# Performance work log

Measured on AMD Instinct MI355X. Metric: run time of the kernel, lower is better.

The kernel has to match this reference:

```python
import jax, jax.numpy as jnp
import numpy as np

B, CIN, H, W = 16, 256, 56, 56
D, HEADS, KS, PAD, STRIDE, M = 256, 8, 3, 1, 1, 4
K = KS * KS
N = D // HEADS
# relative_indices: sum of window coords, flattened row-major, values in [0, 2*KS-2]
REL = (np.arange(KS)[:, None] + np.arange(KS)[None, :]).reshape(-1)


def setup_inputs() -> dict:
    key = jax.random.key(0)
    ks = jax.random.split(key, 7)
    return {
        "x": jax.random.normal(ks[0], (B, CIN, H, W), jnp.float32),
        "q": jax.random.normal(ks[1], (B, D, 1), jnp.float32),
        "Wk": jax.random.normal(ks[2], (D, CIN), jnp.float32) * 0.05,
        "Wv": jax.random.normal(ks[3], (D, CIN), jnp.float32) * 0.05,
        "pos_emb": jax.random.normal(ks[4], (1, 2 * KS - 1), jnp.float32),
        "Wlin": jax.random.normal(ks[5], (1, M), jnp.float32),
        "Wproj": jax.random.normal(ks[6], (D, D), jnp.float32) * 0.05,
    }


def _unfold(t):
    # torch nn.Unfold: (B,C,H,W) -> (B, C*K, L); patches feature dim ordered (C, kh, kw)
    p = jax.lax.conv_general_dilated_patches(
        t, (KS, KS), (STRIDE, STRIDE), [(PAD, PAD), (PAD, PAD)])
    b, _, ho, wo = p.shape
    return p.reshape(b, -1, ho * wo), ho, wo


def reference(x, q, Wk, Wv, pos_emb, Wlin, Wproj):
    b = x.shape[0]
    k = jnp.einsum('oc,bchw->bohw', Wk, x)  # 1x1 conv, no bias
    v = jnp.einsum('oc,bchw->bohw', Wv, x)
    ku, ho, wo = _unfold(k)
    vu, _, _ = _unfold(v)
    L = ho * wo
    ku = ku.reshape(b, HEADS, N, K, L)  # (b, h, n, k, l)
    vu = vu.reshape(b, HEADS, N, K, L)
    qh = q.reshape(b, HEADS, N)  # learned per-batch query, d=1 squeezed
    attn = jnp.einsum('bhn,bhnkl->bhlk', qh, ku)  # (b,h,l,K)
    attn = attn + pos_emb[0, REL]  # relative position bias, shape (K,)
    attn = jax.nn.softmax(attn, axis=-1)
    # repeat d(=1) -> m identical rows then Linear(m,1,no bias): equals scale by sum(Wlin)
    attn = attn * jnp.sum(Wlin)
    out = jnp.einsum('bhlk,bhnkl->bhnl', attn, vu)  # (b,h,n,l)
    out = out.reshape(b, D, ho, wo)  # fold with kernel 1 == reshape
    return jnp.einsum('oc,bchw->bohw', Wproj, out)  # 1x1 proj conv
```

## Files before the change

### kernel.cpp

```cpp
#include <hip/hip_runtime.h>

#define B_     16
#define D_     256
#define HEADS_ 8
#define N_     32
#define H_     56
#define W_     56
#define L_     3136
#define BL_    (B_ * L_)

typedef short short8 __attribute__((ext_vector_type(8)));
typedef float f32x4  __attribute__((ext_vector_type(4)));

__device__ __forceinline__ unsigned short f2bf(float f) {
    union { float f; unsigned u; } c; c.f = f;
    unsigned u = c.u;
    u += 0x7fffu + ((u >> 16) & 1u);
    return (unsigned short)(u >> 16);
}

#define GL2L(g, l) __builtin_amdgcn_global_load_lds( \
    (const __attribute__((address_space(1))) void*)(g), \
    (__attribute__((address_space(3))) void*)(l), 16, 0, 0)

__global__ __launch_bounds__(256) void convert_w_kernel(
    const float* __restrict__ Wv, const float* __restrict__ Wproj,
    const float* __restrict__ Wk, const float* __restrict__ q,
    unsigned short* __restrict__ Wvb, unsigned short* __restrict__ Wpb,
    float* __restrict__ qt)
{
    if (blockIdx.y < 2) {
        const float* src   = (blockIdx.y == 0) ? Wv  : Wproj;
        unsigned short* dst = (blockIdx.y == 0) ? Wvb : Wpb;
        const int i = (blockIdx.x * 256 + threadIdx.x) * 4;
        float4 v = *(const float4*)(src + i);
        uint2 o;
        o.x = (unsigned)f2bf(v.x) | ((unsigned)f2bf(v.y) << 16);
        o.y = (unsigned)f2bf(v.z) | ((unsigned)f2bf(v.w) << 16);
        *(uint2*)(dst + i) = o;
    } else {
        const int b  = blockIdx.x >> 2;
        const int h0 = (blockIdx.x & 3) * 2;
        const int c  = threadIdx.x;
#pragma unroll
        for (int hh = 0; hh < 2; ++hh) {
            const int h = h0 + hh;
            const float* qb = q  + b * D_ + h * N_;
            const float* wr = Wk + (size_t)(h * N_) * D_ + c;
            float acc = 0.f;
#pragma unroll 8
            for (int n = 0; n < N_; ++n)
                acc = fmaf(qb[n], wr[(size_t)n * D_], acc);
            qt[((size_t)b * HEADS_ + h) * D_ + c] = acc;
        }
    }
}

__global__ __launch_bounds__(256) void transpose_s_kernel(
    const float* __restrict__ x, const float* __restrict__ qt,
    unsigned short* __restrict__ Xt, float* __restrict__ S)
{
    __shared__ float tile[64][65];
    __shared__ float qs[2048];
    __shared__ float Sred[4][8][64];

    const int bb = blockIdx.z;
    const int l0 = blockIdx.x * 64;
    const int t  = threadIdx.x;
    const int g4 = (t & 15) * 4;
    const int rr = t >> 4;
    const int sl = t & 63;
    const int cq = t >> 6;

    {
        const float4* s4 = (const float4*)(qt + (size_t)bb * HEADS_ * D_);
        ((float4*)qs)[t]       = s4[t];
        ((float4*)qs)[t + 256] = s4[t + 256];
    }

    float sacc[8];
#pragma unroll
    for (int h = 0; h < 8; ++h) sacc[h] = 0.f;

    const float* xb = x + ((size_t)bb * D_) * L_ + l0;
    unsigned short* Xb = Xt + ((size_t)bb * L_ + l0) * D_;

    for (int ct = 0; ct < 4; ++ct) {
        const int c0 = ct * 64;
        float4 v[4];
#pragma unroll
        for (int i = 0; i < 4; ++i)
            v[i] = *(const float4*)(xb + (size_t)(c0 + rr + i * 16) * L_ + g4);
        __syncthreads();
#pragma unroll
        for (int i = 0; i < 4; ++i)
            *(float4*)&tile[rr + i * 16][g4] = v[i];
        __syncthreads();

#pragma unroll
        for (int i = 0; i < 4; ++i) {
            const int l = rr + i * 16;
            uint2 o;
            o.x = (unsigned)f2bf(tile[g4 + 0][l]) | ((unsigned)f2bf(tile[g4 + 1][l]) << 16);
            o.y = (unsigned)f2bf(tile[g4 + 2][l]) | ((unsigned)f2bf(tile[g4 + 3][l]) << 16);
            *(uint2*)(Xb + (size_t)l * D_ + c0 + g4) = o;
        }

#pragma unroll
        for (int cc = 0; cc < 16; ++cc) {
            const float xv = tile[cq * 16 + cc][sl];
            const int  ci = c0 + cq * 16 + cc;
#pragma unroll
            for (int h = 0; h < 8; ++h)
                sacc[h] = fmaf(qs[h * 256 + ci], xv, sacc[h]);
        }
    }

    __syncthreads();
#pragma unroll
    for (int h = 0; h < 8; ++h) Sred[cq][h][sl] = sacc[h];
    __syncthreads();
    {
        const int h0 = t >> 6;
#pragma unroll
        for (int r = 0; r < 2; ++r) {
            const int h = h0 + r * 4;
            const float s = Sred[0][h][sl] + Sred[1][h][sl] + Sred[2][h][sl] + Sred[3][h][sl];
            S[((size_t)bb * HEADS_ + h) * L_ + l0 + sl] = s;
        }
    }
}

__global__ __launch_bounds__(256) void gemm_v_mfma(
    const unsigned short* __restrict__ Xt, const unsigned short* __restrict__ Wvb,
    unsigned short* __restrict__ Vo)
{
    __shared__ unsigned short As[2][128 * 32];
    __shared__ unsigned short Bs[2][128 * 32];

    const int t = threadIdx.x;
    const int w = t >> 6, lane = t & 63, col = lane & 15, quad = lane >> 4;
    const int wr = w >> 1, wc = w & 1;
    const int n0 = blockIdx.x * 128;
    const int d0 = blockIdx.y * 128;
    const int srow = t >> 2;
    const int skc  = (t & 3) * 8;

    const unsigned short* Ag = Wvb + (size_t)(d0 + srow) * D_ + skc;
    const unsigned short* Bg = Xt + (size_t)(n0 + srow) * D_ + skc;

    f32x4 acc[4][4];
#pragma unroll
    for (int m = 0; m < 4; ++m)
#pragma unroll
        for (int n = 0; n < 4; ++n) acc[m][n] = (f32x4){0.f, 0.f, 0.f, 0.f};

    {
        char* An = (char*)&As[0][0] + w * 1024;
        char* Bn = (char*)&Bs[0][0] + w * 1024;
        GL2L(Ag, An);            GL2L(Ag + 64 * D_, An + 4096);
        GL2L(Bg, Bn);            GL2L(Bg + 64 * D_, Bn + 4096);
    }
    __syncthreads();

#pragma unroll
    for (int kt = 0; kt < 8; ++kt) {
        const int cur = kt & 1;
        if (kt < 7) {
            const int c1 = (kt + 1) * 32;
            char* An = (char*)&As[cur ^ 1][0] + w * 1024;
            char* Bn = (char*)&Bs[cur ^ 1][0] + w * 1024;
            GL2L(Ag + c1, An);           GL2L(Ag + 64 * D_ + c1, An + 4096);
            GL2L(Bg + c1, Bn);           GL2L(Bg + 64 * D_ + c1, Bn + 4096);
        }
        const unsigned short* Ab = &As[cur][0];
        const unsigned short* Bb = &Bs[cur][0];
        short8 af[4], bf[4];
#pragma unroll
        for (int m = 0; m < 4; ++m)
            af[m] = *(const short8*)(Ab + (wr * 64 + m * 16 + col) * 32 + quad * 8);
#pragma unroll
        for (int n = 0; n < 4; ++n)
            bf[n] = *(const short8*)(Bb + (wc * 64 + n * 16 + col) * 32 + quad * 8);
#pragma unroll
        for (int m = 0; m < 4; ++m)
#pragma unroll
            for (int n = 0; n < 4; ++n)
                acc[m][n] = __builtin_amdgcn_mfma_f32_16x16x32_bf16(af[m], bf[n], acc[m][n], 0, 0, 0);
        __syncthreads();
    }

#pragma unroll
    for (int n = 0; n < 4; ++n) {
        const unsigned flat = n0 + wc * 64 + n * 16 + col;
        const unsigned bq = flat / L_;
        const unsigned lq = flat - bq * L_;
        unsigned short* vout = Vo + (size_t)bq * D_ * L_ + lq;
#pragma unroll
        for (int m = 0; m < 4; ++m) {
            const int dbase = d0 + wr * 64 + m * 16 + quad * 4;
#pragma unroll
            for (int r = 0; r < 4; ++r)
                vout[(size_t)(dbase + r) * L_] = f2bf(acc[m][n][r]);
        }
    }
}

__global__ __launch_bounds__(256) void attend_kernel(
    const float* __restrict__ S, const unsigned short* __restrict__ Vo,
    const float* __restrict__ pos_emb, const float* __restrict__ Wlin,
    unsigned short* __restrict__ Om)
{
    __shared__ unsigned short Vs[10][60][8];
    __shared__ float Ss[10][58];

    const int band = blockIdx.x;
    const int half = blockIdx.y;
    const int bh   = blockIdx.z;
    const int y0   = band * 8;
    const int t    = threadIdx.x;

    const float* Sb = S + (size_t)bh * L_;
    for (int wi = t; wi < 580; wi += 256) {
        const int row = wi / 58, c = wi - row * 58;
        const int gr = y0 - 1 + row, gc = c - 1;
        float v = 0.f;
        if (gr >= 0 && gr < H_ && gc >= 0 && gc < W_)
            v = Sb[gr * W_ + gc];
        Ss[row][c] = v;
    }

    const unsigned short* Vbase = Vo + ((size_t)bh * N_ + half * 8) * L_;
    for (int j = t; j < 560; j += 256) {
        const int ch = j & 7;
        const int rr = j >> 3;
        const int row = rr / 7, cg = rr - row * 7;
        const int gr = y0 - 1 + row;
        uint4 v = make_uint4(0u, 0u, 0u, 0u);
        if (gr >= 0 && gr < H_)
            v = *(const uint4*)(Vbase + (size_t)ch * L_ + gr * W_ + cg * 8);
        const unsigned short* hw = (const unsigned short*)&v;
        const int colb = cg * 8 + 1;
#pragma unroll
        for (int i = 0; i < 8; ++i)
            Vs[row][colb + i][ch] = hw[i];
    }
    if (t < 160) {
        const int row = t >> 4, side = (t >> 3) & 1, ch = t & 7;
        Vs[row][side ? 57 : 0][ch] = 0;
    }
    __syncthreads();

    const float scale = Wlin[0] + Wlin[1] + Wlin[2] + Wlin[3];
    const float pe0 = pos_emb[0], pe1 = pos_emb[1], pe2 = pos_emb[2];
    const float pe3 = pos_emb[3], pe4 = pos_emb[4];
    const float bias[9] = {pe0, pe1, pe2, pe1, pe2, pe3, pe2, pe3, pe4};

    for (int p = t; p < 448; p += 256) {
        const int yl = p / 56, xx = p - yl * 56;
        const int lr = yl + 1, lc = xx + 1;

        float lg[9], m = -1e30f;
#pragma unroll
        for (int dy = 0; dy < 3; ++dy)
#pragma unroll
            for (int dx = 0; dx < 3; ++dx) {
                const int k = dy * 3 + dx;
                lg[k] = Ss[lr - 1 + dy][lc - 1 + dx] + bias[k];
                m = fmaxf(m, lg[k]);
            }
        float ssum = 0.f;
#pragma unroll
        for (int k = 0; k < 9; ++k) { lg[k] = __expf(lg[k] - m); ssum += lg[k]; }
        const float inv = scale / ssum;

        float om[8] = {0.f, 0.f, 0.f, 0.f, 0.f, 0.f, 0.f, 0.f};
#pragma unroll
        for (int dy = 0; dy < 3; ++dy)
#pragma unroll
            for (int dx = 0; dx < 3; ++dx) {
                const float wk = lg[dy * 3 + dx] * inv;
                const uint4 v = *(const uint4*)&Vs[lr - 1 + dy][lc - 1 + dx][0];
                const unsigned* u = (const unsigned*)&v;
#pragma unroll
                for (int i = 0; i < 4; ++i) {
                    union { unsigned uu; float f; } lo, hi;
                    lo.uu = u[i] << 16;
                    hi.uu = u[i] & 0xffff0000u;
                    om[2 * i]     = fmaf(wk, lo.f, om[2 * i]);
                    om[2 * i + 1] = fmaf(wk, hi.f, om[2 * i + 1]);
                }
            }

        unsigned short ob[8];
#pragma unroll
        for (int i = 0; i < 8; ++i) ob[i] = f2bf(om[i]);
        const int l = (y0 + yl) * W_ + xx;
        *(uint4*)(Om + ((size_t)bh * L_ + l) * N_ + half * 8) = *(const uint4*)ob;
    }
}

__global__ __launch_bounds__(256) void gemm_proj_mfma(
    const unsigned short* __restrict__ Om, const unsigned short* __restrict__ Wpb,
    float* __restrict__ Out)
{
    __shared__ unsigned short As[2][128 * 32];
    __shared__ unsigned short Bs[2][128 * 32];

    const int t = threadIdx.x;
    const int w = t >> 6, lane = t & 63, col = lane & 15, quad = lane >> 4;
    const int wr = w >> 1, wc = w & 1;
    const int n0 = blockIdx.x * 128;
    const int d0 = blockIdx.y * 128;
    const int srow = t >> 2;
    const int skc  = (t & 3) * 8;

    const unsigned short* Ag = Wpb + (size_t)(d0 + srow) * D_ + skc;
    const int f0 = n0 + srow;
    const unsigned b0q = (unsigned)f0 / L_, l0q = (unsigned)f0 - b0q * L_;
    const int f1 = f0 + 64;
    const unsigned b1q = (unsigned)f1 / L_, l1q = (unsigned)f1 - b1q * L_;
    const unsigned short* Bg0 = Om + ((size_t)(b0q * HEADS_) * L_ + l0q) * N_ + skc;
    const unsigned short* Bg1 = Om + ((size_t)(b1q * HEADS_) * L_ + l1q) * N_ + skc;
    const size_t kstride = (size_t)L_ * N_;

    f32x4 acc[4][4];
#pragma unroll
    for (int m = 0; m < 4; ++m)
#pragma unroll
        for (int n = 0; n < 4; ++n) acc[m][n] = (f32x4){0.f, 0.f, 0.f, 0.f};

    {
        char* An = (char*)&As[0][0] + w * 1024;
        char* Bn = (char*)&Bs[0][0] + w * 1024;
        GL2L(Ag, An);            GL2L(Ag + 64 * D_, An + 4096);
        GL2L(Bg0, Bn);           GL2L(Bg1, Bn + 4096);
    }
    __syncthreads();

#pragma unroll
    for (int kt = 0; kt < 8; ++kt) {
        const int cur = kt & 1;
        if (kt < 7) {
            const int c1 = (kt + 1) * 32;
            char* An = (char*)&As[cur ^ 1][0] + w * 1024;
            char* Bn = (char*)&Bs[cur ^ 1][0] + w * 1024;
            GL2L(Ag + c1, An);                     GL2L(Ag + 64 * D_ + c1, An + 4096);
            GL2L(Bg0 + (kt + 1) * kstride, Bn);    GL2L(Bg1 + (kt + 1) * kstride, Bn + 4096);
        }
        const unsigned short* Ab = &As[cur][0];
        const unsigned short* Bb = &Bs[cur][0];
        short8 af[4], bf[4];
#pragma unroll
        for (int m = 0; m < 4; ++m)
            af[m] = *(const short8*)(Ab + (wr * 64 + m * 16 + col) * 32 + quad * 8);
#pragma unroll
        for (int n = 0; n < 4; ++n)
            bf[n] = *(const short8*)(Bb + (wc * 64 + n * 16 + col) * 32 + quad * 8);
#pragma unroll
        for (int m = 0; m < 4; ++m)
#pragma unroll
            for (int n = 0; n < 4; ++n)
                acc[m][n] = __builtin_amdgcn_mfma_f32_16x16x32_bf16(af[m], bf[n], acc[m][n], 0, 0, 0);
        __syncthreads();
    }

#pragma unroll
    for (int n = 0; n < 4; ++n) {
        const unsigned flat = n0 + wc * 64 + n * 16 + col;
        const unsigned bq = flat / L_;
        const unsigned lq = flat - bq * L_;
        float* oout = Out + (size_t)bq * D_ * L_ + lq;
#pragma unroll
        for (int m = 0; m < 4; ++m) {
            const int dbase = d0 + wr * 64 + m * 16 + quad * 4;
#pragma unroll
            for (int r = 0; r < 4; ++r)
                oout[(size_t)(dbase + r) * L_] = acc[m][n][r];
        }
    }
}

extern "C" void kernel_launch(void* const* d_in, const int* in_sizes, int n_in,
                              void* d_out, int out_size, void* d_ws, size_t ws_size,
                              hipStream_t stream)
{
    const float* x       = (const float*)d_in[0];
    const float* q       = (const float*)d_in[1];
    const float* Wk      = (const float*)d_in[2];
    const float* Wv      = (const float*)d_in[3];
    const float* pos_emb = (const float*)d_in[4];
    const float* Wlin    = (const float*)d_in[5];
    const float* Wproj   = (const float*)d_in[6];
    float* out = (float*)d_out;

    const size_t planeE = (size_t)B_ * D_ * L_;
    unsigned short* Xt  = (unsigned short*)d_ws;
    unsigned short* Vo  = Xt + planeE;
    unsigned short* Om  = Vo + planeE;
    unsigned short* Wvb = Om + planeE;
    unsigned short* Wpb = Wvb + D_ * D_;
    float*          S   = (float*)(Wpb + D_ * D_);
    float*          qt  = S + (size_t)B_ * HEADS_ * L_;

    convert_w_kernel<<<dim3(64, 3), 256, 0, stream>>>(Wv, Wproj, Wk, q, Wvb, Wpb, qt);
    transpose_s_kernel<<<dim3(49, 1, 16), 256, 0, stream>>>(x, qt, Xt, S);
    gemm_v_mfma<<<dim3(BL_ / 128, 2), 256, 0, stream>>>(Xt, Wvb, Vo);
    attend_kernel<<<dim3(7, 4, B_ * HEADS_), 256, 0, stream>>>(S, Vo, pos_emb, Wlin, Om);
    gemm_proj_mfma<<<dim3(BL_ / 128, 2), 256, 0, stream>>>(Om, Wpb, out);
}
```

Before: 196.2 us.

## Split transpose and score kernels; store V channel-last per head for vector loads

```diff
diff --git a/kernel.cpp b/kernel.cpp
--- a/kernel.cpp
+++ b/kernel.cpp
@@ -56,19 +56,46 @@
     }
 }
 
-__global__ __launch_bounds__(256) void transpose_s_kernel(
-    const float* __restrict__ x, const float* __restrict__ qt,
-    unsigned short* __restrict__ Xt, float* __restrict__ S)
+__global__ __launch_bounds__(256) void transpose_x_kernel(
+    const float* __restrict__ x, unsigned short* __restrict__ Xt)
 {
     __shared__ float tile[64][65];
-    __shared__ float qs[2048];
-    __shared__ float Sred[4][8][64];
-
     const int bb = blockIdx.z;
+    const int c0 = blockIdx.y * 64;
     const int l0 = blockIdx.x * 64;
     const int t  = threadIdx.x;
     const int g4 = (t & 15) * 4;
     const int rr = t >> 4;
+
+    const float* xb = x + ((size_t)bb * D_ + c0) * L_ + l0;
+#pragma unroll
+    for (int i = 0; i < 4; ++i) {
+        const int c = rr + i * 16;
+        float4 v = *(const float4*)(xb + (size_t)c * L_ + g4);
+        *(float4*)&tile[c][g4] = v;
+    }
+    __syncthreads();
+    unsigned short* Xb = Xt + ((size_t)bb * L_ + l0) * D_ + c0;
+#pragma unroll
+    for (int i = 0; i < 4; ++i) {
+        const int l = rr + i * 16;
+        uint2 o;
+        o.x = (unsigned)f2bf(tile[g4 + 0][l]) | ((unsigned)f2bf(tile[g4 + 1][l]) << 16);
+        o.y = (unsigned)f2bf(tile[g4 + 2][l]) | ((unsigned)f2bf(tile[g4 + 3][l]) << 16);
+        *(uint2*)(Xb + (size_t)l * D_ + g4) = o;
+    }
+}
+
+__global__ __launch_bounds__(256) void s_kernel(
+    const float* __restrict__ x, const float* __restrict__ qt,
+    float* __restrict__ S)
+{
+    __shared__ float qs[HEADS_ * D_];
+    __shared__ float red[4][HEADS_][64];
+
+    const int bb = blockIdx.y;
+    const int l0 = blockIdx.x * 64;
+    const int t  = threadIdx.x;
     const int sl = t & 63;
     const int cq = t >> 6;
 
@@ -77,57 +104,31 @@
         ((float4*)qs)[t]       = s4[t];
         ((float4*)qs)[t + 256] = s4[t + 256];
     }
+    __syncthreads();
 
     float sacc[8];
 #pragma unroll
     for (int h = 0; h < 8; ++h) sacc[h] = 0.f;
 
-    const float* xb = x + ((size_t)bb * D_) * L_ + l0;
-    unsigned short* Xb = Xt + ((size_t)bb * L_ + l0) * D_;
-
-    for (int ct = 0; ct < 4; ++ct) {
-        const int c0 = ct * 64;
-        float4 v[4];
-#pragma unroll
-        for (int i = 0; i < 4; ++i)
-            v[i] = *(const float4*)(xb + (size_t)(c0 + rr + i * 16) * L_ + g4);
-        __syncthreads();
-#pragma unroll
-        for (int i = 0; i < 4; ++i)
-            *(float4*)&tile[rr + i * 16][g4] = v[i];
-        __syncthreads();
-
-#pragma unroll
-        for (int i = 0; i < 4; ++i) {
-            const int l = rr + i * 16;
-            uint2 o;
-            o.x = (unsigned)f2bf(tile[g4 + 0][l]) | ((unsigned)f2bf(tile[g4 + 1][l]) << 16);
-            o.y = (unsigned)f2bf(tile[g4 + 2][l]) | ((unsigned)f2bf(tile[g4 + 3][l]) << 16);
-            *(uint2*)(Xb + (size_t)l * D_ + c0 + g4) = o;
-        }
-
-#pragma unroll
-        for (int cc = 0; cc < 16; ++cc) {
-            const float xv = tile[cq * 16 + cc][sl];
-            const int  ci = c0 + cq * 16 + cc;
-#pragma unroll
-            for (int h = 0; h < 8; ++h)
-                sacc[h] = fmaf(qs[h * 256 + ci], xv, sacc[h]);
-        }
-    }
-
-    __syncthreads();
-#pragma unroll
-    for (int h = 0; h < 8; ++h) Sred[cq][h][sl] = sacc[h];
-    __syncthreads();
-    {
-        const int h0 = t >> 6;
-#pragma unroll
-        for (int r = 0; r < 2; ++r) {
-            const int h = h0 + r * 4;
-            const float s = Sred[0][h][sl] + Sred[1][h][sl] + Sred[2][h][sl] + Sred[3][h][sl];
-            S[((size_t)bb * HEADS_ + h) * L_ + l0 + sl] = s;
-        }
+    const float* xb = x + (size_t)bb * D_ * L_ + l0 + sl;
+#pragma unroll 4
+    for (int c = cq * 64; c < cq * 64 + 64; ++c) {
+        const float xv = xb[(size_t)c * L_];
+#pragma unroll
+        for (int h = 0; h < 8; ++h)
+            sacc[h] = fmaf(qs[h * D_ + c], xv, sacc[h]);
+    }
+
+#pragma unroll
+    for (int h = 0; h < 8; ++h) red[cq][h][sl] = sacc[h];
+    __syncthreads();
+
+    const int h0 = t >> 6;
+#pragma unroll
+    for (int r = 0; r < 2; ++r) {
+        const int h = h0 + r * 4;
+        const float s = red[0][h][sl] + red[1][h][sl] + red[2][h][sl] + red[3][h][sl];
+        S[((size_t)bb * HEADS_ + h) * L_ + l0 + sl] = s;
     }
 }
 
@@ -195,13 +196,16 @@
         const unsigned flat = n0 + wc * 64 + n * 16 + col;
         const unsigned bq = flat / L_;
         const unsigned lq = flat - bq * L_;
-        unsigned short* vout = Vo + (size_t)bq * D_ * L_ + lq;
 #pragma unroll
         for (int m = 0; m < 4; ++m) {
-            const int dbase = d0 + wr * 64 + m * 16 + quad * 4;
-#pragma unroll
-            for (int r = 0; r < 4; ++r)
-                vout[(size_t)(dbase + r) * L_] = f2bf(acc[m][n][r]);
+            const int d  = d0 + wr * 64 + m * 16 + quad * 4;
+            const int h  = d >> 5;
+            const int dn = d & 31;
+            unsigned short ob[4];
+#pragma unroll
+            for (int r = 0; r < 4; ++r) ob[r] = f2bf(acc[m][n][r]);
+            *(uint2*)(Vo + ((size_t)(bq * HEADS_ + h) * L_ + lq) * N_ + dn) =
+                *(const uint2*)ob;
         }
     }
 }
@@ -211,7 +215,7 @@
     const float* __restrict__ pos_emb, const float* __restrict__ Wlin,
     unsigned short* __restrict__ Om)
 {
-    __shared__ unsigned short Vs[10][60][8];
+    __shared__ __align__(16) unsigned short Vs[10][60][8];
     __shared__ float Ss[10][58];
 
     const int band = blockIdx.x;
@@ -230,24 +234,14 @@
         Ss[row][c] = v;
     }
 
-    const unsigned short* Vbase = Vo + ((size_t)bh * N_ + half * 8) * L_;
-    for (int j = t; j < 560; j += 256) {
-        const int ch = j & 7;
-        const int rr = j >> 3;
-        const int row = rr / 7, cg = rr - row * 7;
-        const int gr = y0 - 1 + row;
+    const unsigned short* Vbase = Vo + (size_t)bh * L_ * N_ + half * 8;
+    for (int wi = t; wi < 580; wi += 256) {
+        const int row = wi / 58, c = wi - row * 58;
+        const int gr = y0 - 1 + row, gc = c - 1;
         uint4 v = make_uint4(0u, 0u, 0u, 0u);
-        if (gr >= 0 && gr < H_)
-            v = *(const uint4*)(Vbase + (size_t)ch * L_ + gr * W_ + cg * 8);
-        const unsigned short* hw = (const unsigned short*)&v;
-        const int colb = cg * 8 + 1;
-#pragma unroll
-        for (int i = 0; i < 8; ++i)
-            Vs[row][colb + i][ch] = hw[i];
-    }
-    if (t < 160) {
-        const int row = t >> 4, side = (t >> 3) & 1, ch = t & 7;
-        Vs[row][side ? 57 : 0][ch] = 0;
+        if (gr >= 0 && gr < H_ && gc >= 0 && gc < W_)
+            v = *(const uint4*)(Vbase + (size_t)(gr * W_ + gc) * N_);
+        *(uint4*)&Vs[row][c][0] = v;
     }
     __syncthreads();
 
@@ -404,7 +398,8 @@
     float*          qt  = S + (size_t)B_ * HEADS_ * L_;
 
     convert_w_kernel<<<dim3(64, 3), 256, 0, stream>>>(Wv, Wproj, Wk, q, Wvb, Wpb, qt);
-    transpose_s_kernel<<<dim3(49, 1, 16), 256, 0, stream>>>(x, qt, Xt, S);
+    transpose_x_kernel<<<dim3(L_ / 64, D_ / 64, B_), 256, 0, stream>>>(x, Xt);
+    s_kernel<<<dim3(L_ / 64, B_), 256, 0, stream>>>(x, qt, S);
     gemm_v_mfma<<<dim3(BL_ / 128, 2), 256, 0, stream>>>(Xt, Wvb, Vo);
     attend_kernel<<<dim3(7, 4, B_ * HEADS_), 256, 0, stream>>>(S, Vo, pos_emb, Wlin, Om);
     gemm_proj_mfma<<<dim3(BL_ / 128, 2), 256, 0, stream>>>(Om, Wpb, out);
```

Result: faster. 191.1 us (-2.6%).
